# Optimization experiments

Hardware: AMD Instinct MI355X
Metric: run time of the kernel (lower is better)

Reference implementation:

```python
import jax, jax.numpy as jnp
import numpy as np

B, SD, AD, H, QE, NQ = 16384, 512, 64, 1024, 64, 64


def setup_inputs() -> dict:
    key = jax.random.key(0)
    ks = jax.random.split(key, 12)
    s = 0.02
    p = lambda k, shape: (jax.random.normal(k, shape, jnp.float32) * s)
    return {
        "state": jax.random.normal(ks[0], (B, SD), jnp.float32),
        "action": jax.random.normal(ks[1], (B, AD), jnp.float32),
        # twin critics: leading axis 2 stacks q1 / q2 parameters
        "W_e1": p(ks[2], (2, QE, 1)),      "b_e1": p(ks[3], (2, QE)),
        "W_e2": p(ks[4], (2, QE, QE)),     "b_e2": p(ks[5], (2, QE)),
        "W_f1": p(ks[6], (2, H, SD + AD)), "b_f1": p(ks[7], (2, H)),
        "g1": jnp.ones((2, H), jnp.float32),  "beta1": jnp.zeros((2, H), jnp.float32),
        "W_f2": p(ks[8], (2, H, H)),       "b_f2": p(ks[9], (2, H)),
        "g2": jnp.ones((2, H), jnp.float32),  "beta2": jnp.zeros((2, H), jnp.float32),
        "W_h": p(ks[10], (2, 1, H + QE)),  "b_h": p(ks[11], (2, 1)),
    }


def _layernorm(x, g, b, eps=1e-5):
    mu = x.mean(-1, keepdims=True)
    var = ((x - mu) ** 2).mean(-1, keepdims=True)
    return (x - mu) * jax.lax.rsqrt(var + eps) * g + b


def _qnet(state, action, W_e1, b_e1, W_e2, b_e2, W_f1, b_f1, g1, beta1,
          W_f2, b_f2, g2, beta2, W_h, b_h):
    # feature_net (eval mode: dropout is identity)
    x = jnp.concatenate([state, action], axis=-1)            # [B, SD+AD]
    h = jax.nn.relu(_layernorm(x @ W_f1.T + b_f1, g1, beta1))
    feat = jax.nn.relu(_layernorm(h @ W_f2.T + b_f2, g2, beta2))  # [B, H]
    # tau embedding (batch-independent -> compute once per quantile, not per sample)
    tau = (jnp.linspace(0.0, 1.0, NQ + 1)[:-1] + 1.0 / (2 * NQ))[:, None]  # [NQ,1]
    te = jax.nn.relu(tau @ W_e1.T + b_e1) @ W_e2.T + b_e2    # [NQ, QE]
    # head on concat([feat, te]) == linear split (exact same math as the 64-iter loop)
    q_feat = feat @ W_h[0, :H]                               # [B]
    q_tau = te @ W_h[0, H:]                                  # [NQ]
    return q_feat[:, None] + q_tau[None, :] + b_h[0]         # [B, NQ]


def reference(state, action, W_e1, b_e1, W_e2, b_e2, W_f1, b_f1, g1, beta1,
              W_f2, b_f2, g2, beta2, W_h, b_h):
    qnet = lambda *ps: _qnet(state, action, *ps)
    q = jax.vmap(qnet)(W_e1, b_e1, W_e2, b_e2, W_f1, b_f1, g1, beta1,
                       W_f2, b_f2, g2, beta2, W_h, b_h)      # [2, B, NQ]
    return q[0], q[1]
```

## Files before the change

kernel.cpp:

```cpp
#include <hip/hip_runtime.h>
#include <stdint.h>

#define BATCH 16384
#define SDIM 512
#define ADIM 64
#define XDIM 576
#define HDIM 1024
#define NQD 64
#define QED 64

typedef __attribute__((ext_vector_type(8))) short short8;
typedef __attribute__((ext_vector_type(4))) float f32x4;

static __device__ inline unsigned short f2bf(float f) {
  unsigned int u = __float_as_uint(f);
  unsigned int r = (u + 0x7fffu + ((u >> 16) & 1u)) >> 16;
  return (unsigned short)r;
}
static __device__ inline float bf2f(unsigned short u) {
  return __uint_as_float(((unsigned int)u) << 16);
}

static __device__ inline void gload_lds16(const void* g, void* l) {
  __builtin_amdgcn_global_load_lds(
      (const __attribute__((address_space(1))) uint32_t*)g,
      (__attribute__((address_space(3))) uint32_t*)l, 16, 0, 0);
}


__global__ __launch_bounds__(256) void cvt_x(const float* __restrict__ st,
                                             const float* __restrict__ ac,
                                             unsigned short* __restrict__ xb) {
  const int total = BATCH * XDIM / 4;
  for (int i = blockIdx.x * blockDim.x + threadIdx.x; i < total;
       i += gridDim.x * blockDim.x) {
    const int e = i * 4;
    const int b = e / XDIM;
    const int j = e - b * XDIM;
    float4 v;
    if (j < SDIM) v = *(const float4*)(st + (size_t)b * SDIM + j);
    else          v = *(const float4*)(ac + (size_t)b * ADIM + (j - SDIM));
    ushort4 o;
    o.x = f2bf(v.x); o.y = f2bf(v.y); o.z = f2bf(v.z); o.w = f2bf(v.w);
    ((ushort4*)xb)[i] = o;
  }
}

__global__ __launch_bounds__(256) void cvt_w2(const float* __restrict__ s1,
                                              unsigned short* __restrict__ d1, int n1,
                                              const float* __restrict__ s2,
                                              unsigned short* __restrict__ d2, int n2) {
  for (int i = blockIdx.x * blockDim.x + threadIdx.x; i < n1 + n2;
       i += gridDim.x * blockDim.x) {
    const float4 v = (i < n1) ? ((const float4*)s1)[i] : ((const float4*)s2)[i - n1];
    ushort4 o;
    o.x = f2bf(v.x); o.y = f2bf(v.y); o.z = f2bf(v.z); o.w = f2bf(v.w);
    if (i < n1) ((ushort4*)d1)[i] = o; else ((ushort4*)d2)[i - n1] = o;
  }
}


__global__ void qtau_kernel(const float* __restrict__ We1, const float* __restrict__ be1,
                            const float* __restrict__ We2, const float* __restrict__ be2,
                            const float* __restrict__ Wh,  const float* __restrict__ bh,
                            float* __restrict__ qtau) {
  const int c = blockIdx.x >> 6;
  const int nq = blockIdx.x & 63;
  const int q = threadIdx.x;
  const float tau = (float)nq / 64.0f + 0.0078125f;
  float acc = be2[c * 64 + q];
  for (int e = 0; e < 64; ++e) {
    const float t1 = fmaxf(tau * We1[c * 64 + e] + be1[c * 64 + e], 0.0f);
    acc += t1 * We2[(c * 64 + q) * 64 + e];
  }
  float v = acc * Wh[c * (HDIM + QED) + HDIM + q];
  #pragma unroll
  for (int off = 32; off; off >>= 1) v += __shfl_xor(v, off);
  if (q == 0) qtau[c * 64 + nq] = v + bh[c];
}


template <int K>
__global__ __launch_bounds__(256, 3) void gemm128(const unsigned short* __restrict__ A,
                                                  const unsigned short* __restrict__ W,
                                                  const float* __restrict__ bias,
                                                  unsigned short* __restrict__ C) {
  constexpr int BK = 32;
  constexpr int NT = K / BK;
  __shared__ unsigned short As[2][128 * BK];
  __shared__ unsigned short Ws[2][128 * BK];

  const int tid  = threadIdx.x;
  const int lane = tid & 63;
  const int wave = tid >> 6;
  const int wm = wave >> 1;
  const int wn = wave & 1;

  const int bid = (int)blockIdx.x;
  const int logical = (bid & 7) * 128 + (bid >> 3);
  const int mBase = (logical >> 3) * 128;
  const int nBase = (logical & 7) * 128;

  const int srow  = tid >> 2;
  const int sslot = tid & 3;

  f32x4 acc[4][4];
  #pragma unroll
  for (int m = 0; m < 4; ++m)
    #pragma unroll
    for (int n = 0; n < 4; ++n) {
      f32x4 z = {0.f, 0.f, 0.f, 0.f};
      acc[m][n] = z;
    }

  auto stage = [&](int b, int kt) {
    const unsigned short* Ag = A + (size_t)mBase * K + (size_t)kt * BK;
    const unsigned short* Wg = W + (size_t)nBase * K + (size_t)kt * BK;
    #pragma unroll
    for (int i = 0; i < 2; ++i) {
      const int r = i * 64 + srow;
      gload_lds16(Ag + (size_t)r * K + sslot * 8, &As[b][(i * 64 + wave * 16) * BK]);
      gload_lds16(Wg + (size_t)r * K + sslot * 8, &Ws[b][(i * 64 + wave * 16) * BK]);
    }
  };

  stage(0, 0);
  __syncthreads();

  int buf = 0;
  for (int kt = 0; kt < NT; ++kt) {
    if (kt + 1 < NT) stage(buf ^ 1, kt + 1);
    short8 af[4], bfr[4];
    #pragma unroll
    for (int m = 0; m < 4; ++m) {
      const int r = wm * 64 + m * 16 + (lane & 15);
      af[m] = *(const short8*)&As[buf][r * BK + (lane >> 4) * 8];
    }
    #pragma unroll
    for (int n = 0; n < 4; ++n) {
      const int r = wn * 64 + n * 16 + (lane & 15);
      bfr[n] = *(const short8*)&Ws[buf][r * BK + (lane >> 4) * 8];
    }
    #pragma unroll
    for (int m = 0; m < 4; ++m)
      #pragma unroll
      for (int n = 0; n < 4; ++n)
        acc[m][n] = __builtin_amdgcn_mfma_f32_16x16x32_bf16(af[m], bfr[n], acc[m][n], 0, 0, 0);
    __syncthreads();
    buf ^= 1;
  }

  #pragma unroll
  for (int m = 0; m < 4; ++m) {
    const int r0 = mBase + wm * 64 + m * 16 + (lane >> 4) * 4;
    #pragma unroll
    for (int n = 0; n < 4; ++n) {
      const int col = nBase + wn * 64 + n * 16 + (lane & 15);
      const float bv = bias[col];
      #pragma unroll
      for (int j = 0; j < 4; ++j)
        C[(size_t)(r0 + j) * HDIM + col] = f2bf(acc[m][n][j] + bv);
    }
  }
}


template <bool HEAD>
__global__ __launch_bounds__(256) void ln_head(const unsigned short* __restrict__ X,
                                               const float* __restrict__ g,
                                               const float* __restrict__ bta,
                                               unsigned short* __restrict__ Y,
                                               const float* __restrict__ Wh,
                                               const float* __restrict__ qt,
                                               float* __restrict__ out) {
  const int b = blockIdx.x;
  const int tid = threadIdx.x;
  const int lane = tid & 63;
  const int wave = tid >> 6;
  __shared__ float rs_[4], rq_[4], rp_[4];

  const ushort4 xv = ((const ushort4*)(X + (size_t)b * HDIM))[tid];
  const float x0 = bf2f(xv.x), x1 = bf2f(xv.y), x2 = bf2f(xv.z), x3 = bf2f(xv.w);
  float s = x0 + x1 + x2 + x3;
  float q = x0 * x0 + x1 * x1 + x2 * x2 + x3 * x3;
  #pragma unroll
  for (int off = 32; off; off >>= 1) {
    s += __shfl_xor(s, off);
    q += __shfl_xor(q, off);
  }
  if (lane == 0) { rs_[wave] = s; rq_[wave] = q; }
  __syncthreads();
  s = rs_[0] + rs_[1] + rs_[2] + rs_[3];
  q = rq_[0] + rq_[1] + rq_[2] + rq_[3];
  const float mu = s * (1.0f / 1024.0f);
  const float var = q * (1.0f / 1024.0f) - mu * mu;
  const float rsig = rsqrtf(var + 1e-5f);

  const float4 gv = ((const float4*)g)[tid];
  const float4 bv = ((const float4*)bta)[tid];
  const float y0 = fmaxf((x0 - mu) * rsig * gv.x + bv.x, 0.0f);
  const float y1 = fmaxf((x1 - mu) * rsig * gv.y + bv.y, 0.0f);
  const float y2 = fmaxf((x2 - mu) * rsig * gv.z + bv.z, 0.0f);
  const float y3 = fmaxf((x3 - mu) * rsig * gv.w + bv.w, 0.0f);

  if constexpr (!HEAD) {
    ushort4 o;
    o.x = f2bf(y0); o.y = f2bf(y1); o.z = f2bf(y2); o.w = f2bf(y3);
    ((ushort4*)(Y + (size_t)b * HDIM))[tid] = o;
  } else {
    const float4 wv = ((const float4*)Wh)[tid];
    float p = y0 * wv.x + y1 * wv.y + y2 * wv.z + y3 * wv.w;
    #pragma unroll
    for (int off = 32; off; off >>= 1) p += __shfl_xor(p, off);
    if (lane == 0) rp_[wave] = p;
    __syncthreads();
    if (tid < 64) {
      const float qf = rp_[0] + rp_[1] + rp_[2] + rp_[3];
      out[(size_t)b * NQD + tid] = qf + qt[tid];
    }
  }
}


extern "C" void kernel_launch(void* const* d_in, const int* in_sizes, int n_in,
                              void* d_out, int out_size, void* d_ws, size_t ws_size,
                              hipStream_t stream) {
  (void)in_sizes; (void)n_in; (void)out_size; (void)ws_size;
  const float* state  = (const float*)d_in[0];
  const float* action = (const float*)d_in[1];
  const float* We1 = (const float*)d_in[2];
  const float* be1 = (const float*)d_in[3];
  const float* We2 = (const float*)d_in[4];
  const float* be2 = (const float*)d_in[5];
  const float* Wf1 = (const float*)d_in[6];
  const float* bW1 = (const float*)d_in[7];
  const float* g1  = (const float*)d_in[8];
  const float* bt1 = (const float*)d_in[9];
  const float* Wf2 = (const float*)d_in[10];
  const float* bW2 = (const float*)d_in[11];
  const float* g2  = (const float*)d_in[12];
  const float* bt2 = (const float*)d_in[13];
  const float* Wh  = (const float*)d_in[14];
  const float* bh  = (const float*)d_in[15];
  float* out = (float*)d_out;

  char* ws = (char*)d_ws;
  unsigned short* xb   = (unsigned short*)(ws);
  unsigned short* w1b  = (unsigned short*)(ws + 18874368);
  unsigned short* w2b  = (unsigned short*)(ws + 21233664);
  float*          qtw  = (float*)(ws + 25427968);
  unsigned short* ha   = (unsigned short*)(ws + 25428480);
  unsigned short* hb   = (unsigned short*)(ws + 58982912);

  cvt_x<<<2048, 256, 0, stream>>>(state, action, xb);
  cvt_w2<<<2048, 256, 0, stream>>>(Wf1, w1b, 2 * HDIM * XDIM / 4,
                                   Wf2, w2b, 2 * HDIM * HDIM / 4);
  qtau_kernel<<<128, 64, 0, stream>>>(We1, be1, We2, be2, Wh, bh, qtw);

  for (int c = 0; c < 2; ++c) {
    gemm128<XDIM><<<1024, 256, 0, stream>>>(
        xb, w1b + (size_t)c * HDIM * XDIM, bW1 + c * HDIM, ha);
    ln_head<false><<<BATCH, 256, 0, stream>>>(
        ha, g1 + c * HDIM, bt1 + c * HDIM, hb, nullptr, nullptr, nullptr);
    gemm128<HDIM><<<1024, 256, 0, stream>>>(
        hb, w2b + (size_t)c * HDIM * HDIM, bW2 + c * HDIM, ha);
    ln_head<true><<<BATCH, 256, 0, stream>>>(
        ha, g2 + c * HDIM, bt2 + c * HDIM, nullptr,
        Wh + (size_t)c * (HDIM + QED), qtw + c * 64, out + (size_t)c * BATCH * NQD);
  }
}
```

Baseline: 224.4 us.

## Replace 128x128 GEMM with 256x256 four-stage ring-buffered swizzled-LDS kernel

Rewrites both feature GEMMs to use 256x256 output tiles per 512-thread block. Tiles are staged through a 4-deep LDS ring with three K-slices kept in flight, paced by explicit vmcnt waits and raw barriers instead of double buffering with __syncthreads. LDS rows get an XOR swizzle to avoid bank conflicts, and the MFMA loop runs at raised wave priority. The larger tiles cut global traffic per FLOP. In exchange, only 256 blocks are launched, LDS use reaches 128KB per block, and register pressure from 32 accumulators per wave is high.

```diff
diff --git a/kernel.cpp b/kernel.cpp
--- a/kernel.cpp
+++ b/kernel.cpp
@@ -26,6 +26,8 @@
       (const __attribute__((address_space(1))) uint32_t*)g,
       (__attribute__((address_space(3))) uint32_t*)l, 16, 0, 0);
 }
+
+#define FENCE() asm volatile("" ::: "memory")
 
 
 __global__ __launch_bounds__(256) void cvt_x(const float* __restrict__ st,
@@ -81,85 +83,105 @@
 
 
 template <int K>
-__global__ __launch_bounds__(256, 3) void gemm128(const unsigned short* __restrict__ A,
-                                                  const unsigned short* __restrict__ W,
-                                                  const float* __restrict__ bias,
-                                                  unsigned short* __restrict__ C) {
-  constexpr int BK = 32;
-  constexpr int NT = K / BK;
-  __shared__ unsigned short As[2][128 * BK];
-  __shared__ unsigned short Ws[2][128 * BK];
+__global__ __launch_bounds__(512, 2) void gemm_ring(const unsigned short* __restrict__ A,
+                                                    const unsigned short* __restrict__ W,
+                                                    const float* __restrict__ bias,
+                                                    unsigned short* __restrict__ C) {
+  constexpr int NT = K / 32;
+  __shared__ unsigned short As[4][256][32];
+  __shared__ unsigned short Bs[4][256][32];
 
   const int tid  = threadIdx.x;
   const int lane = tid & 63;
   const int wave = tid >> 6;
-  const int wm = wave >> 1;
-  const int wn = wave & 1;
+  const int wm = wave >> 2;
+  const int wn = wave & 3;
 
   const int bid = (int)blockIdx.x;
-  const int logical = (bid & 7) * 128 + (bid >> 3);
-  const int mBase = (logical >> 3) * 128;
-  const int nBase = (logical & 7) * 128;
-
-  const int srow  = tid >> 2;
-  const int sslot = tid & 3;
-
-  f32x4 acc[4][4];
-  #pragma unroll
-  for (int m = 0; m < 4; ++m)
-    #pragma unroll
-    for (int n = 0; n < 4; ++n) {
+  const int logical = (bid & 7) * 32 + (bid >> 3);
+  const int mBase = (logical >> 2) * 256;
+  const int nBase = (logical & 3) * 256;
+
+  auto stage = [&](int ring, int kt) {
+    #pragma unroll
+    for (int i = 0; i < 2; ++i) {
+      const int flat = i * 512 + tid;
+      const int row  = flat >> 2;
+      const int ps   = flat & 3;
+      const int ls   = ps ^ ((row >> 1) & 3);
+      gload_lds16(A + (size_t)(mBase + row) * K + kt * 32 + ls * 8,
+                  &As[ring][0][0] + (size_t)flat * 8);
+      gload_lds16(W + (size_t)(nBase + row) * K + kt * 32 + ls * 8,
+                  &Bs[ring][0][0] + (size_t)flat * 8);
+    }
+  };
+
+  f32x4 acc[8][4];
+  #pragma unroll
+  for (int fm = 0; fm < 8; ++fm)
+    #pragma unroll
+    for (int fn = 0; fn < 4; ++fn) {
       f32x4 z = {0.f, 0.f, 0.f, 0.f};
-      acc[m][n] = z;
-    }
-
-  auto stage = [&](int b, int kt) {
-    const unsigned short* Ag = A + (size_t)mBase * K + (size_t)kt * BK;
-    const unsigned short* Wg = W + (size_t)nBase * K + (size_t)kt * BK;
-    #pragma unroll
-    for (int i = 0; i < 2; ++i) {
-      const int r = i * 64 + srow;
-      gload_lds16(Ag + (size_t)r * K + sslot * 8, &As[b][(i * 64 + wave * 16) * BK]);
-      gload_lds16(Wg + (size_t)r * K + sslot * 8, &Ws[b][(i * 64 + wave * 16) * BK]);
-    }
-  };
+      acc[fm][fn] = z;
+    }
 
   stage(0, 0);
-  __syncthreads();
-
-  int buf = 0;
-  for (int kt = 0; kt < NT; ++kt) {
-    if (kt + 1 < NT) stage(buf ^ 1, kt + 1);
-    short8 af[4], bfr[4];
-    #pragma unroll
-    for (int m = 0; m < 4; ++m) {
-      const int r = wm * 64 + m * 16 + (lane & 15);
-      af[m] = *(const short8*)&As[buf][r * BK + (lane >> 4) * 8];
-    }
-    #pragma unroll
-    for (int n = 0; n < 4; ++n) {
-      const int r = wn * 64 + n * 16 + (lane & 15);
-      bfr[n] = *(const short8*)&Ws[buf][r * BK + (lane >> 4) * 8];
-    }
-    #pragma unroll
-    for (int m = 0; m < 4; ++m)
+  if (NT > 1) stage(1, 1);
+  if (NT > 2) stage(2, 2);
+  FENCE();
+  if (NT > 2)      asm volatile("s_waitcnt vmcnt(8)" ::: "memory");
+  else if (NT > 1) asm volatile("s_waitcnt vmcnt(4)" ::: "memory");
+  else             asm volatile("s_waitcnt vmcnt(0)" ::: "memory");
+  __builtin_amdgcn_s_barrier();
+  FENCE();
+
+  for (int t = 0; t < NT; ++t) {
+    const int ring = t & 3;
+    if (t + 3 < NT) stage((t + 3) & 3, t + 3);
+
+    short8 af[8], bf[4];
+    #pragma unroll
+    for (int fm = 0; fm < 8; ++fm) {
+      const int r  = wm * 128 + fm * 16 + (lane & 15);
+      const int ps = (lane >> 4) ^ ((r >> 1) & 3);
+      af[fm] = *(const short8*)&As[ring][r][ps * 8];
+    }
+    #pragma unroll
+    for (int fn = 0; fn < 4; ++fn) {
+      const int r  = wn * 64 + fn * 16 + (lane & 15);
+      const int ps = (lane >> 4) ^ ((r >> 1) & 3);
+      bf[fn] = *(const short8*)&Bs[ring][r][ps * 8];
+    }
+
+    __builtin_amdgcn_s_setprio(1);
+    #pragma unroll
+    for (int fm = 0; fm < 8; ++fm)
       #pragma unroll
-      for (int n = 0; n < 4; ++n)
-        acc[m][n] = __builtin_amdgcn_mfma_f32_16x16x32_bf16(af[m], bfr[n], acc[m][n], 0, 0, 0);
-    __syncthreads();
-    buf ^= 1;
-  }
-
-  #pragma unroll
-  for (int m = 0; m < 4; ++m) {
-    const int r0 = mBase + wm * 64 + m * 16 + (lane >> 4) * 4;
-    #pragma unroll
-    for (int n = 0; n < 4; ++n) {
-      const int col = nBase + wn * 64 + n * 16 + (lane & 15);
+      for (int fn = 0; fn < 4; ++fn)
+        acc[fm][fn] = __builtin_amdgcn_mfma_f32_16x16x32_bf16(af[fm], bf[fn],
+                                                              acc[fm][fn], 0, 0, 0);
+    __builtin_amdgcn_s_setprio(0);
+
+    if (t + 1 < NT) {
+      FENCE();
+      if (t + 3 < NT)      asm volatile("s_waitcnt vmcnt(8)" ::: "memory");
+      else if (t + 2 < NT) asm volatile("s_waitcnt vmcnt(4)" ::: "memory");
+      else                 asm volatile("s_waitcnt vmcnt(0)" ::: "memory");
+      __builtin_amdgcn_s_barrier();
+      FENCE();
+    }
+  }
+
+  #pragma unroll
+  for (int fm = 0; fm < 8; ++fm) {
+    const int r0 = mBase + wm * 128 + fm * 16 + (lane >> 4) * 4;
+    #pragma unroll
+    for (int fn = 0; fn < 4; ++fn) {
+      const int col = nBase + wn * 64 + fn * 16 + (lane & 15);
       const float bv = bias[col];
       #pragma unroll
       for (int j = 0; j < 4; ++j)
-        C[(size_t)(r0 + j) * HDIM + col] = f2bf(acc[m][n][j] + bv);
+        C[(size_t)(r0 + j) * HDIM + col] = f2bf(acc[fm][fn][j] + bv);
     }
   }
 }
@@ -258,11 +280,11 @@
   qtau_kernel<<<128, 64, 0, stream>>>(We1, be1, We2, be2, Wh, bh, qtw);
 
   for (int c = 0; c < 2; ++c) {
-    gemm128<XDIM><<<1024, 256, 0, stream>>>(
+    gemm_ring<XDIM><<<256, 512, 0, stream>>>(
         xb, w1b + (size_t)c * HDIM * XDIM, bW1 + c * HDIM, ha);
     ln_head<false><<<BATCH, 256, 0, stream>>>(
         ha, g1 + c * HDIM, bt1 + c * HDIM, hb, nullptr, nullptr, nullptr);
-    gemm128<HDIM><<<1024, 256, 0, stream>>>(
+    gemm_ring<HDIM><<<256, 512, 0, stream>>>(
         hb, w2b + (size_t)c * HDIM * HDIM, bW2 + c * HDIM, ha);
     ln_head<true><<<BATCH, 256, 0, stream>>>(
         ha, g2 + c * HDIM, bt2 + c * HDIM, nullptr,
```

New measurement: 233.0 us. 3.8% more time.
